# Optimization experiments

Measured on AMD Instinct MI355X. Metric: run time of the kernel, lower is better.

## Reference

```python
import jax, jax.numpy as jnp
import numpy as np

N, F, H, NB = 32768, 1024, 64, 6  # tokens, features, update_hidden, num branches


def setup_inputs() -> dict:
    key = jax.random.key(0)
    kx, k1, k2 = jax.random.split(key, 3)
    s1 = (2.0 / F) ** 0.5  # Linear init scale: sqrt(2/in_features)
    s2 = (2.0 / H) ** 0.5
    x = jax.random.normal(kx, (N, F), dtype=jnp.float32)
    W1 = jax.random.normal(k1, (NB, F, H), dtype=jnp.float32) * s1  # fc1 of [mk,mv,mq,meta,malpha,mmemory]
    B1 = jnp.zeros((NB, H), dtype=jnp.float32)
    W2 = jax.random.normal(k2, (NB, H, F), dtype=jnp.float32) * s2
    B2 = jnp.zeros((NB, F), dtype=jnp.float32)
    return {"x": x, "W1": W1, "B1": B1, "W2": W2, "B2": B2}


def _mlp(x, w1, b1, w2, b2):
    # MemoryMLP: x + fc2(relu(fc1(x)))
    h = jax.nn.relu(x @ w1 + b1)
    return x + h @ w2 + b2


def reference(x, W1, B1, W2, B2):
    # Branches 0..4 (mk, mv, mq, meta, malpha) all take x: batch them in one pass.
    h = jax.nn.relu(jnp.einsum('nf,mfh->mnh', x, W1[:5]) + B1[:5, None, :])  # [5,N,H]
    y = x[None] + jnp.einsum('mnh,mhf->mnf', h, W2[:5]) + B2[:5, None, :]   # [5,N,F]
    k, v, q = y[0], y[1], y[2]
    eta = jax.nn.softplus(y[3])
    alpha = jax.nn.sigmoid(y[4])
    # mmemory takes q; forward output = x + memory
    memory = _mlp(q, W1[5], B1[5], W2[5], B2[5])
    out = x + memory
    # Stack all six live signals so every branch is exercised: [6,N,F]
    return jnp.stack([k, v, q, eta, alpha, out], axis=0)
```

## Files before the change

kernel.cpp:

```cpp
#include <hip/hip_runtime.h>
#include <math.h>

#define N_TOK 32768
#define F_DIM 1024
#define H_DIM 64

typedef __attribute__((ext_vector_type(8))) short short8;
typedef __attribute__((ext_vector_type(4))) short short4v;
typedef __attribute__((ext_vector_type(4))) float floatx4;

__device__ __forceinline__ short f2bf(float f) {
  unsigned u = __builtin_bit_cast(unsigned, f);
  unsigned r = (u + 0x7fffu + ((u >> 16) & 1u)) >> 16;
  return (short)r;
}

__device__ __forceinline__ float softplusf(float v) {
  float a = fabsf(v);
  float r = log1pf(expf(-a));
  return v > 0.f ? v + r : r;
}

__global__ void prep_weights(const float* __restrict__ W1, const float* __restrict__ W2,
                             short* __restrict__ w1t, short* __restrict__ w2t) {
  int idx = blockIdx.x * blockDim.x + threadIdx.x;
  if (idx >= 6 * 64 * 1024) return;
  {
    int f = idx & 1023;
    int mh = idx >> 10;
    int h = mh & 63;
    int m = mh >> 6;
    w1t[idx] = f2bf(W1[(m * 1024 + f) * 64 + h]);
  }
  {
    int h = idx & 63;
    int mf = idx >> 6;
    int f = mf & 1023;
    int m = mf >> 10;
    w2t[idx] = f2bf(W2[(m * 64 + h) * 1024 + f]);
  }
}

#define XQ_STRIDE 1048
__global__ __launch_bounds__(256, 3) void k_fused(
    const float* __restrict__ x, const short* __restrict__ w1t,
    const float* __restrict__ b1, const short* __restrict__ w2t,
    const float* __restrict__ b2, const short* __restrict__ w1t5,
    const float* __restrict__ b1_5, const short* __restrict__ w2t5,
    const float* __restrict__ b2_5, float* __restrict__ out) {
  __shared__ short xq[16 * XQ_STRIDE];
  __shared__ short hlds[16 * 328];

  const int tid = threadIdx.x;
  const int lane = tid & 63;
  const int wid = tid >> 6;
  const int m16 = lane & 15;
  const int quad = lane >> 4;
  const int row0 = blockIdx.x * 16;

  for (int pass = 0; pass < 4; pass++) {
    const int r = pass * 4 + wid;
    const float* xr = x + (size_t)(row0 + r) * F_DIM;
#pragma unroll
    for (int j = 0; j < 2; j++) {
      const int c = j * 512 + lane * 8;
      float4 va = *(const float4*)(xr + c);
      float4 vb = *(const float4*)(xr + c + 4);
      short8 p = {f2bf(va.x), f2bf(va.y), f2bf(va.z), f2bf(va.w),
                  f2bf(vb.x), f2bf(vb.y), f2bf(vb.z), f2bf(vb.w)};
      *(short8*)(&xq[r * XQ_STRIDE + c]) = p;
    }
  }
  __syncthreads();

  floatx4 acc[5];
#pragma unroll
  for (int i = 0; i < 5; i++) acc[i] = (floatx4){0.f, 0.f, 0.f, 0.f};

  {
    const short* xrow = &xq[m16 * XQ_STRIDE];
    const short* w1c = w1t + (size_t)wid * 80 * 1024;
    for (int kk = 0; kk < 32; kk++) {
      const int k0 = kk * 32 + quad * 8;
      short8 a = *(const short8*)(xrow + k0);
#pragma unroll
      for (int ct = 0; ct < 5; ct++) {
        short8 w = *(const short8*)(w1c + (ct * 16 + m16) * 1024 + k0);
        acc[ct] = __builtin_amdgcn_mfma_f32_16x16x32_bf16(w, a, acc[ct], 0, 0, 0);
      }
    }
  }

#pragma unroll
  for (int ct = 0; ct < 5; ct++) {
    const int c0 = wid * 80 + ct * 16 + quad * 4;
    const float4 bias = *(const float4*)(b1 + c0);
    short4v p = {f2bf(fmaxf(acc[ct][0] + bias.x, 0.f)),
                 f2bf(fmaxf(acc[ct][1] + bias.y, 0.f)),
                 f2bf(fmaxf(acc[ct][2] + bias.z, 0.f)),
                 f2bf(fmaxf(acc[ct][3] + bias.w, 0.f))};
    *(short4v*)(&hlds[m16 * 328 + c0]) = p;
  }
  __syncthreads();

  short8 ha[5], hb[5];
#pragma unroll
  for (int b = 0; b < 5; b++) {
    const short* hr = &hlds[m16 * 328 + b * 64];
    ha[b] = *(const short8*)(hr + quad * 8);
    hb[b] = *(const short8*)(hr + 32 + quad * 8);
  }

  const size_t gr = (size_t)row0 + m16;
  const float* xr = x + gr * F_DIM;

  for (int ct = 0; ct < 16; ct++) {
    const int col = wid * 256 + ct * 16 + quad * 4;
    const int wrow = wid * 256 + ct * 16 + m16;
    floatx4 xv = *(const floatx4*)(xr + col);
#pragma unroll
    for (int b = 0; b < 5; b++) {
      const short* wb = w2t + (size_t)b * (F_DIM * H_DIM) + (size_t)wrow * 64;
      short8 w0 = *(const short8*)(wb + quad * 8);
      short8 w1v = *(const short8*)(wb + 32 + quad * 8);
      floatx4 c = {0.f, 0.f, 0.f, 0.f};
      c = __builtin_amdgcn_mfma_f32_16x16x32_bf16(w0, ha[b], c, 0, 0, 0);
      c = __builtin_amdgcn_mfma_f32_16x16x32_bf16(w1v, hb[b], c, 0, 0, 0);
      floatx4 b2v = *(const floatx4*)(b2 + b * F_DIM + col);
      float y0 = c[0] + xv[0] + b2v[0];
      float y1 = c[1] + xv[1] + b2v[1];
      float y2 = c[2] + xv[2] + b2v[2];
      float y3 = c[3] + xv[3] + b2v[3];
      if (b == 3) {
        y0 = softplusf(y0); y1 = softplusf(y1);
        y2 = softplusf(y2); y3 = softplusf(y3);
      } else if (b == 4) {
        y0 = 1.f / (1.f + expf(-y0)); y1 = 1.f / (1.f + expf(-y1));
        y2 = 1.f / (1.f + expf(-y2)); y3 = 1.f / (1.f + expf(-y3));
      }
      floatx4 y = {y0, y1, y2, y3};
      float* op = out + (size_t)b * N_TOK * F_DIM + gr * F_DIM + col;
      if (b == 2) {
        *(floatx4*)op = y;
        short4v qp = {f2bf(y0), f2bf(y1), f2bf(y2), f2bf(y3)};
        *(short4v*)(&xq[m16 * XQ_STRIDE + col]) = qp;
      } else {
        __builtin_nontemporal_store(y, (floatx4*)op);
      }
    }
  }
  __syncthreads();

  {
    floatx4 acc5 = {0.f, 0.f, 0.f, 0.f};
    const short* qrow = &xq[m16 * XQ_STRIDE];
    const short* w5 = w1t5 + (size_t)(wid * 16 + m16) * 1024;
    for (int kk = 0; kk < 32; kk++) {
      const int k0 = kk * 32 + quad * 8;
      short8 qf = *(const short8*)(qrow + k0);
      short8 w = *(const short8*)(w5 + k0);
      acc5 = __builtin_amdgcn_mfma_f32_16x16x32_bf16(w, qf, acc5, 0, 0, 0);
    }
    const int c0 = wid * 16 + quad * 4;
    const float4 bias = *(const float4*)(b1_5 + c0);
    short4v p = {f2bf(fmaxf(acc5[0] + bias.x, 0.f)),
                 f2bf(fmaxf(acc5[1] + bias.y, 0.f)),
                 f2bf(fmaxf(acc5[2] + bias.z, 0.f)),
                 f2bf(fmaxf(acc5[3] + bias.w, 0.f))};
    *(short4v*)(&hlds[m16 * 72 + c0]) = p;
  }
  __syncthreads();

  {
    short8 ha5 = *(const short8*)(&hlds[m16 * 72 + quad * 8]);
    short8 hb5 = *(const short8*)(&hlds[m16 * 72 + 32 + quad * 8]);
    const float* qr = out + (size_t)2 * N_TOK * F_DIM + gr * F_DIM;
    float* o5 = out + (size_t)5 * N_TOK * F_DIM + gr * F_DIM;
    for (int ct = 0; ct < 16; ct++) {
      const int col = wid * 256 + ct * 16 + quad * 4;
      const int wrow = wid * 256 + ct * 16 + m16;
      const short* wb = w2t5 + (size_t)wrow * 64;
      short8 w0 = *(const short8*)(wb + quad * 8);
      short8 w1v = *(const short8*)(wb + 32 + quad * 8);
      floatx4 c = {0.f, 0.f, 0.f, 0.f};
      c = __builtin_amdgcn_mfma_f32_16x16x32_bf16(w0, ha5, c, 0, 0, 0);
      c = __builtin_amdgcn_mfma_f32_16x16x32_bf16(w1v, hb5, c, 0, 0, 0);
      floatx4 xv = *(const floatx4*)(xr + col);
      floatx4 qv = *(const floatx4*)(qr + col);
      floatx4 b2v = *(const floatx4*)(b2_5 + col);
      floatx4 y = {c[0] + xv[0] + qv[0] + b2v[0],
                   c[1] + xv[1] + qv[1] + b2v[1],
                   c[2] + xv[2] + qv[2] + b2v[2],
                   c[3] + xv[3] + qv[3] + b2v[3]};
      __builtin_nontemporal_store(y, (floatx4*)(o5 + col));
    }
  }
}

extern "C" void kernel_launch(void* const* d_in, const int* in_sizes, int n_in,
                              void* d_out, int out_size, void* d_ws, size_t ws_size,
                              hipStream_t stream) {
  const float* x = (const float*)d_in[0];
  const float* W1 = (const float*)d_in[1];
  const float* B1 = (const float*)d_in[2];
  const float* W2 = (const float*)d_in[3];
  const float* B2 = (const float*)d_in[4];
  float* out = (float*)d_out;

  short* w1t = (short*)d_ws;
  short* w2t = w1t + 6 * 64 * 1024;

  prep_weights<<<(6 * 64 * 1024 + 255) / 256, 256, 0, stream>>>(W1, W2, w1t, w2t);

  k_fused<<<N_TOK / 16, 256, 0, stream>>>(x, w1t, B1, w2t, B2,
                                          w1t + 5 * 64 * 1024, B1 + 5 * 64,
                                          w2t + 5 * 1024 * 64, B2 + 5 * 1024, out);
}
```

Measured before the change: 1.336 ms.

## Use 512-thread blocks and split per-block work across eight waves

The fused kernel goes from 4 to 8 waves per 16-row block. The first-layer 20 column tiles are redistributed as 2–3 tiles per wave, second-layer output columns are split into 8 groups of 128, and the branch-5 hidden GEMM runs on only four waves. With LDS per block unchanged, this is meant to raise resident waves per CU so more memory and MFMA work is in flight. The aggressive launch-bounds hint may squeeze the register budget and cause spills, and waves 4–7 sit idle during the branch-5 hidden GEMM.

```diff
diff --git a/kernel.cpp b/kernel.cpp
--- a/kernel.cpp
+++ b/kernel.cpp
@@ -42,7 +42,7 @@
 }
 
 #define XQ_STRIDE 1048
-__global__ __launch_bounds__(256, 3) void k_fused(
+__global__ __launch_bounds__(512, 6) void k_fused(
     const float* __restrict__ x, const short* __restrict__ w1t,
     const float* __restrict__ b1, const short* __restrict__ w2t,
     const float* __restrict__ b2, const short* __restrict__ w1t5,
@@ -58,8 +58,9 @@
   const int quad = lane >> 4;
   const int row0 = blockIdx.x * 16;
 
-  for (int pass = 0; pass < 4; pass++) {
-    const int r = pass * 4 + wid;
+#pragma unroll
+  for (int rr = 0; rr < 2; rr++) {
+    const int r = wid * 2 + rr;
     const float* xr = x + (size_t)(row0 + r) * F_DIM;
 #pragma unroll
     for (int j = 0; j < 2; j++) {
@@ -73,32 +74,46 @@
   }
   __syncthreads();
 
-  floatx4 acc[5];
-#pragma unroll
-  for (int i = 0; i < 5; i++) acc[i] = (floatx4){0.f, 0.f, 0.f, 0.f};
+  floatx4 acc0 = {0.f, 0.f, 0.f, 0.f};
+  floatx4 acc1 = {0.f, 0.f, 0.f, 0.f};
+  floatx4 acc2 = {0.f, 0.f, 0.f, 0.f};
+  const int t0 = wid, t1 = wid + 8, t2 = wid + 16;
+  const bool has3 = (wid < 4);
 
   {
     const short* xrow = &xq[m16 * XQ_STRIDE];
-    const short* w1c = w1t + (size_t)wid * 80 * 1024;
+    const short* w0p = w1t + (size_t)(t0 * 16 + m16) * 1024;
+    const short* w1p = w1t + (size_t)(t1 * 16 + m16) * 1024;
+    const short* w2p = w1t + (size_t)(t2 * 16 + m16) * 1024;
     for (int kk = 0; kk < 32; kk++) {
       const int k0 = kk * 32 + quad * 8;
       short8 a = *(const short8*)(xrow + k0);
-#pragma unroll
-      for (int ct = 0; ct < 5; ct++) {
-        short8 w = *(const short8*)(w1c + (ct * 16 + m16) * 1024 + k0);
-        acc[ct] = __builtin_amdgcn_mfma_f32_16x16x32_bf16(w, a, acc[ct], 0, 0, 0);
-      }
-    }
-  }
-
-#pragma unroll
-  for (int ct = 0; ct < 5; ct++) {
-    const int c0 = wid * 80 + ct * 16 + quad * 4;
+      acc0 = __builtin_amdgcn_mfma_f32_16x16x32_bf16(*(const short8*)(w0p + k0), a, acc0, 0, 0, 0);
+      acc1 = __builtin_amdgcn_mfma_f32_16x16x32_bf16(*(const short8*)(w1p + k0), a, acc1, 0, 0, 0);
+      if (has3)
+        acc2 = __builtin_amdgcn_mfma_f32_16x16x32_bf16(*(const short8*)(w2p + k0), a, acc2, 0, 0, 0);
+    }
+  }
+
+  {
+    const int c0 = t0 * 16 + quad * 4;
     const float4 bias = *(const float4*)(b1 + c0);
-    short4v p = {f2bf(fmaxf(acc[ct][0] + bias.x, 0.f)),
-                 f2bf(fmaxf(acc[ct][1] + bias.y, 0.f)),
-                 f2bf(fmaxf(acc[ct][2] + bias.z, 0.f)),
-                 f2bf(fmaxf(acc[ct][3] + bias.w, 0.f))};
+    short4v p = {f2bf(fmaxf(acc0[0] + bias.x, 0.f)), f2bf(fmaxf(acc0[1] + bias.y, 0.f)),
+                 f2bf(fmaxf(acc0[2] + bias.z, 0.f)), f2bf(fmaxf(acc0[3] + bias.w, 0.f))};
+    *(short4v*)(&hlds[m16 * 328 + c0]) = p;
+  }
+  {
+    const int c0 = t1 * 16 + quad * 4;
+    const float4 bias = *(const float4*)(b1 + c0);
+    short4v p = {f2bf(fmaxf(acc1[0] + bias.x, 0.f)), f2bf(fmaxf(acc1[1] + bias.y, 0.f)),
+                 f2bf(fmaxf(acc1[2] + bias.z, 0.f)), f2bf(fmaxf(acc1[3] + bias.w, 0.f))};
+    *(short4v*)(&hlds[m16 * 328 + c0]) = p;
+  }
+  if (has3) {
+    const int c0 = t2 * 16 + quad * 4;
+    const float4 bias = *(const float4*)(b1 + c0);
+    short4v p = {f2bf(fmaxf(acc2[0] + bias.x, 0.f)), f2bf(fmaxf(acc2[1] + bias.y, 0.f)),
+                 f2bf(fmaxf(acc2[2] + bias.z, 0.f)), f2bf(fmaxf(acc2[3] + bias.w, 0.f))};
     *(short4v*)(&hlds[m16 * 328 + c0]) = p;
   }
   __syncthreads();
@@ -114,9 +129,10 @@
   const size_t gr = (size_t)row0 + m16;
   const float* xr = x + gr * F_DIM;
 
-  for (int ct = 0; ct < 16; ct++) {
-    const int col = wid * 256 + ct * 16 + quad * 4;
-    const int wrow = wid * 256 + ct * 16 + m16;
+  for (int ct = 0; ct < 8; ct++) {
+    const int g = wid * 8 + ct;
+    const int col = g * 16 + quad * 4;
+    const int wrow = g * 16 + m16;
     floatx4 xv = *(const floatx4*)(xr + col);
 #pragma unroll
     for (int b = 0; b < 5; b++) {
@@ -151,7 +167,7 @@
   }
   __syncthreads();
 
-  {
+  if (wid < 4) {
     floatx4 acc5 = {0.f, 0.f, 0.f, 0.f};
     const short* qrow = &xq[m16 * XQ_STRIDE];
     const short* w5 = w1t5 + (size_t)(wid * 16 + m16) * 1024;
@@ -176,9 +192,10 @@
     short8 hb5 = *(const short8*)(&hlds[m16 * 72 + 32 + quad * 8]);
     const float* qr = out + (size_t)2 * N_TOK * F_DIM + gr * F_DIM;
     float* o5 = out + (size_t)5 * N_TOK * F_DIM + gr * F_DIM;
-    for (int ct = 0; ct < 16; ct++) {
-      const int col = wid * 256 + ct * 16 + quad * 4;
-      const int wrow = wid * 256 + ct * 16 + m16;
+    for (int ct = 0; ct < 8; ct++) {
+      const int g = wid * 8 + ct;
+      const int col = g * 16 + quad * 4;
+      const int wrow = g * 16 + m16;
       const short* wb = w2t5 + (size_t)wrow * 64;
       short8 w0 = *(const short8*)(wb + quad * 8);
       short8 w1v = *(const short8*)(wb + 32 + quad * 8);
@@ -212,7 +229,7 @@
 
   prep_weights<<<(6 * 64 * 1024 + 255) / 256, 256, 0, stream>>>(W1, W2, w1t, w2t);
 
-  k_fused<<<N_TOK / 16, 256, 0, stream>>>(x, w1t, B1, w2t, B2,
+  k_fused<<<N_TOK / 16, 512, 0, stream>>>(x, w1t, B1, w2t, B2,
                                           w1t + 5 * 64 * 1024, B1 + 5 * 64,
                                           w2t + 5 * 1024 * 64, B2 + 5 * 1024, out);
 }
```

Result: slower. 1.445 ms (+8.2%).
